# Optimization experiments

Hardware: AMD Instinct MI355X
Metric: run time of the kernel (lower is better)

The kernel has to match this reference:

```python
import jax, jax.numpy as jnp
import numpy as np

K = 1024
H = 16
HEAD = K // H

def setup_inputs() -> dict:
    key = jax.random.key(0)
    ks = jax.random.split(key, 6)
    b, t = 2, 2048
    x = jax.random.normal(ks[0], (b, t, K), dtype=jnp.float32)
    padding = jnp.ones((b, t), dtype=jnp.int32)
    s = 1.0 / np.sqrt(K)
    Wq = jax.random.normal(ks[1], (K, K), dtype=jnp.float32) * s
    Wk = jax.random.normal(ks[2], (K, K), dtype=jnp.float32) * s
    Wv = jax.random.normal(ks[3], (K, K), dtype=jnp.float32) * s
    Wo = jax.random.normal(ks[4], (K, K), dtype=jnp.float32) * s
    bo = jnp.zeros((K,), dtype=jnp.float32)
    return {"x": x, "padding": padding, "Wq": Wq, "Wk": Wk, "Wv": Wv, "Wo": Wo, "bo": bo}

def reference(x, padding, Wq, Wk, Wv, Wo, bo):
    b, t, k = x.shape
    h, d = H, HEAD
    # projections (nn.Linear: x @ W.T), then split heads -> [b,h,t,d]
    q = (x @ Wq.T).reshape(b, t, h, d).transpose(0, 2, 1, 3)
    kk = (x @ Wk.T).reshape(b, t, h, d).transpose(0, 2, 1, 3)
    v = (x @ Wv.T).reshape(b, t, h, d).transpose(0, 2, 1, 3)
    scores = jnp.einsum('bhqd,bhkd->bhqk', q, kk)
    # key-side padding mask: positions with padding==0 get -inf (before scaling,
    # same result since -inf/sqrt(d) == -inf)
    mask = (padding == 0)[:, None, None, :]  # [b,1,1,t]
    scores = jnp.where(mask, -jnp.inf, scores) / np.sqrt(d).astype(np.float32)
    weights = jax.nn.softmax(scores, axis=-1)
    out = jnp.einsum('bhqk,bhkd->bhqd', weights, v)
    out = out.transpose(0, 2, 1, 3).reshape(b, t, h * d)
    return out @ Wo.T + bo
```

## Files before the change

### kernel.cpp

```cpp
#include <hip/hip_runtime.h>
#include <cmath>
#include <stdint.h>

#define K_DIM 1024
#define NH    16
#define HD    64
#define T     2048
#define NTOK  4096
#define NBH   32

typedef __bf16 bf16x8 __attribute__((ext_vector_type(8)));
typedef float  f32x4  __attribute__((ext_vector_type(4)));

__device__ __forceinline__ unsigned short f2bf(float f) {
  union { float f; unsigned u; } v; v.f = f;
  unsigned u = v.u;
  return (unsigned short)((u + 0x7FFFu + ((u >> 16) & 1u)) >> 16);
}
__device__ __forceinline__ unsigned short f2bf_hu(float f) {
  union { float f; unsigned u; } v; v.f = f;
  return (unsigned short)((v.u + 0x8000u) >> 16);
}

__device__ __forceinline__ void gload16(const void* g, void* l) {
  __builtin_amdgcn_global_load_lds(
      (__attribute__((address_space(1))) void*)(g),
      (__attribute__((address_space(3))) void*)(l),
      16, 0, 0);
}

__global__ void convert_kernel(const float* __restrict__ x,
                               const float* __restrict__ Wq,
                               const float* __restrict__ Wk,
                               const float* __restrict__ Wv,
                               const float* __restrict__ Wo,
                               unsigned short* __restrict__ xb,
                               unsigned short* __restrict__ wqkv,
                               unsigned short* __restrict__ wob)
{
  const size_t NX = (size_t)NTOK * K_DIM;
  const size_t NW = (size_t)K_DIM * K_DIM;
  size_t i = ((size_t)blockIdx.x * blockDim.x + threadIdx.x) * 4;
  const float* src; unsigned short* dst; size_t off;
  if (i < NX)             { src = x;  dst = xb;          off = i; }
  else if (i < NX + NW)   { src = Wq; dst = wqkv;        off = i - NX; }
  else if (i < NX + 2*NW) { src = Wk; dst = wqkv + NW;   off = i - NX - NW; }
  else if (i < NX + 3*NW) { src = Wv; dst = wqkv + 2*NW; off = i - NX - 2*NW; }
  else                    { src = Wo; dst = wob;         off = i - NX - 3*NW; }
  float4 v = *(const float4*)(src + off);
  ushort4 o;
  o.x = f2bf(v.x); o.y = f2bf(v.y); o.z = f2bf(v.z); o.w = f2bf(v.w);
  *(ushort4*)(dst + off) = o;
}

template <int MODE, int TM, int TN>
__global__ __launch_bounds__(256, 2)
void gemm_bt(const unsigned short* __restrict__ A,
             const unsigned short* __restrict__ B,
             unsigned short* __restrict__ o_q,
             unsigned short* __restrict__ o_k,
             unsigned short* __restrict__ o_v,
             float* __restrict__ o_f,
             const float* __restrict__ bias)
{
  __shared__ unsigned short Asm[TM * 64];
  __shared__ unsigned short Bsm[TN * 64];
  const int tid  = threadIdx.x;
  const int wave = tid >> 6;
  const int lane = tid & 63;
  const int lq   = lane & 15;
  const int quad = lane >> 4;
  const int bm = blockIdx.x, bn = blockIdx.y;
  const int wm = (wave >> 1) * (TM / 2), wn = (wave & 1) * (TN / 2);
  const int MT = TM / 32, NT = TN / 32;

  f32x4 acc[MT][NT];
#pragma unroll
  for (int i = 0; i < MT; ++i)
#pragma unroll
    for (int j = 0; j < NT; ++j) acc[i][j] = (f32x4){0.f, 0.f, 0.f, 0.f};

  const char* Ab = (const char*)(A + (size_t)bm * TM * K_DIM);
  const char* Bb = (const char*)(B + (size_t)bn * TN * K_DIM);

  for (int k0 = 0; k0 < K_DIM; k0 += 64) {
#pragma unroll
    for (int i = 0; i < MT; ++i) {
      int off   = i * 4096 + wave * 1024 + lane * 16;
      int row   = off >> 7;
      int chunk = (off >> 4) & 7;
      int scol  = (chunk ^ (row & 7)) << 4;
      gload16(Ab + (size_t)row * (K_DIM * 2) + (size_t)k0 * 2 + scol,
              (char*)Asm + off - lane * 16);
    }
#pragma unroll
    for (int i = 0; i < NT; ++i) {
      int off   = i * 4096 + wave * 1024 + lane * 16;
      int row   = off >> 7;
      int chunk = (off >> 4) & 7;
      int scol  = (chunk ^ (row & 7)) << 4;
      gload16(Bb + (size_t)row * (K_DIM * 2) + (size_t)k0 * 2 + scol,
              (char*)Bsm + off - lane * 16);
    }
    __syncthreads();
#pragma unroll
    for (int kk = 0; kk < 64; kk += 32) {
      bf16x8 af[MT], bfr[NT];
#pragma unroll
      for (int mt = 0; mt < MT; ++mt) {
        int row = wm + mt * 16 + lq;
        int sw  = (quad + (kk >> 3)) ^ (row & 7);
        af[mt] = *(const bf16x8*)((const char*)Asm + row * 128 + (sw << 4));
      }
#pragma unroll
      for (int nt = 0; nt < NT; ++nt) {
        int row = wn + nt * 16 + lq;
        int sw  = (quad + (kk >> 3)) ^ (row & 7);
        bfr[nt] = *(const bf16x8*)((const char*)Bsm + row * 128 + (sw << 4));
      }
#pragma unroll
      for (int mt = 0; mt < MT; ++mt)
#pragma unroll
        for (int nt = 0; nt < NT; ++nt)
          acc[mt][nt] = __builtin_amdgcn_mfma_f32_16x16x32_bf16(af[mt], bfr[nt], acc[mt][nt], 0, 0, 0);
    }
    __syncthreads();
  }

#pragma unroll
  for (int mt = 0; mt < MT; ++mt) {
    int mbase = bm * TM + wm + mt * 16 + quad * 4;
#pragma unroll
    for (int nt = 0; nt < NT; ++nt) {
      int n = bn * TN + wn + nt * 16 + lq;
      if (MODE == 1) {
        int which = mbase >> 10, c = mbase & 1023;
        int h = c >> 6, d0 = c & 63;
        int b = n >> 11, t = n & 2047;
        if (which < 2) {
          ushort4 pk;
          pk.x = f2bf(acc[mt][nt][0]); pk.y = f2bf(acc[mt][nt][1]);
          pk.z = f2bf(acc[mt][nt][2]); pk.w = f2bf(acc[mt][nt][3]);
          unsigned short* dst = which ? o_k : o_q;
          *(ushort4*)&dst[((size_t)(b * NH + h) * T + t) * HD + d0] = pk;
        } else {
#pragma unroll
          for (int r = 0; r < 4; ++r)
            o_v[((size_t)(b * NH + h) * HD + d0 + r) * T + t] = f2bf(acc[mt][nt][r]);
        }
      } else {
        float4 bv = *(const float4*)&bias[mbase];
        float4 o;
        o.x = acc[mt][nt][0] + bv.x; o.y = acc[mt][nt][1] + bv.y;
        o.z = acc[mt][nt][2] + bv.z; o.w = acc[mt][nt][3] + bv.w;
        *(float4*)&o_f[(size_t)n * K_DIM + mbase] = o;
      }
    }
  }
}

__global__ __launch_bounds__(256, 2)
void attn_kernel(const unsigned short* __restrict__ Q,
                 const unsigned short* __restrict__ Kb,
                 const unsigned short* __restrict__ Vt,
                 const int* __restrict__ padding,
                 unsigned short* __restrict__ O)
{
  __shared__ unsigned short Ksm[128 * 64];
  __shared__ unsigned short Vsm[64 * 128];
  __shared__ unsigned short Plds[4][32 * 32 * 4];

  const int tid  = threadIdx.x;
  const int wave = tid >> 6;
  const int lane = tid & 63;
  const int lq   = lane & 15;
  const int quad = lane >> 4;
  const int qt = blockIdx.x;
  const int bh = blockIdx.y;
  const int b  = bh >> 4;
  const int h  = bh & 15;
  const int qbase = qt * 128 + wave * 32;

  bf16x8 qf[2][2];
#pragma unroll
  for (int nq = 0; nq < 2; ++nq)
#pragma unroll
    for (int kk = 0; kk < 2; ++kk)
      qf[nq][kk] = *(const bf16x8*)&Q[((size_t)bh * T + qbase + nq * 16 + lq) * HD + kk * 32 + quad * 8];

  f32x4 o_acc[4][2];
#pragma unroll
  for (int md = 0; md < 4; ++md)
#pragma unroll
    for (int nq = 0; nq < 2; ++nq) o_acc[md][nq] = (f32x4){0.f, 0.f, 0.f, 0.f};
  float l_part[2] = {0.f, 0.f};

  const float Cs = 0.18033688011112042f;

  for (int kt = 0; kt < T / 128; ++kt) {
#pragma unroll
    for (int i = 0; i < 4; ++i) {
      int off = i * 4096 + wave * 1024 + lane * 16;
      {
        int row = off >> 7, chunk = (off >> 4) & 7;
        int scol = (chunk ^ (row & 7)) << 4;
        gload16((const char*)Kb + ((size_t)(bh * T + kt * 128 + row) * HD) * 2 + scol,
                (char*)Ksm + off - lane * 16);
      }
      {
        int row = off >> 8, chunk = (off >> 4) & 15;
        int scol = (chunk ^ (row & 15)) << 4;
        gload16((const char*)Vt + ((size_t)(bh * HD + row) * T + (size_t)kt * 128) * 2 + scol,
                (char*)Vsm + off - lane * 16);
      }
    }
    __syncthreads();

    f32x4 st[8][2];
#pragma unroll
    for (int nt = 0; nt < 8; ++nt)
#pragma unroll
      for (int nq = 0; nq < 2; ++nq) st[nt][nq] = (f32x4){0.f, 0.f, 0.f, 0.f};
#pragma unroll
    for (int kk = 0; kk < 2; ++kk) {
#pragma unroll
      for (int nt = 0; nt < 8; ++nt) {
        int row = nt * 16 + lq;
        int sw  = (quad + kk * 4) ^ (row & 7);
        bf16x8 kf = *(const bf16x8*)((const char*)Ksm + row * 128 + (sw << 4));
        st[nt][0] = __builtin_amdgcn_mfma_f32_16x16x32_bf16(kf, qf[0][kk], st[nt][0], 0, 0, 0);
        st[nt][1] = __builtin_amdgcn_mfma_f32_16x16x32_bf16(kf, qf[1][kk], st[nt][1], 0, 0, 0);
      }
    }

#pragma unroll
    for (int nt = 0; nt < 8; ++nt) {
      int4 pd = *(const int4*)&padding[b * T + kt * 128 + nt * 16 + quad * 4];
#pragma unroll
      for (int nq = 0; nq < 2; ++nq) {
        float p0 = pd.x ? __builtin_amdgcn_exp2f(st[nt][nq][0] * Cs) : 0.f;
        float p1 = pd.y ? __builtin_amdgcn_exp2f(st[nt][nq][1] * Cs) : 0.f;
        float p2 = pd.z ? __builtin_amdgcn_exp2f(st[nt][nq][2] * Cs) : 0.f;
        float p3 = pd.w ? __builtin_amdgcn_exp2f(st[nt][nq][3] * Cs) : 0.f;
        l_part[nq] += (p0 + p1) + (p2 + p3);
        ushort4 pk;
        pk.x = f2bf_hu(p0); pk.y = f2bf_hu(p1); pk.z = f2bf_hu(p2); pk.w = f2bf_hu(p3);
        int row = nt * 4 + quad;
        int col = nq * 16 + lq;
        *(ushort4*)&Plds[wave][(row * 32 + col) * 4] = pk;
      }
    }
    asm volatile("s_waitcnt lgkmcnt(0)" ::: "memory");

#pragma unroll
    for (int kk = 0; kk < 4; ++kk) {
      bf16x8 pf[2];
#pragma unroll
      for (int nq = 0; nq < 2; ++nq) {
        int row0 = kk * 8 + quad * 2;
        ushort4 lo = *(const ushort4*)&Plds[wave][((row0    ) * 32 + nq * 16 + lq) * 4];
        ushort4 hi = *(const ushort4*)&Plds[wave][((row0 + 1) * 32 + nq * 16 + lq) * 4];
        union { ushort4 u[2]; bf16x8 v; } cvt;
        cvt.u[0] = lo; cvt.u[1] = hi;
        pf[nq] = cvt.v;
      }
#pragma unroll
      for (int md = 0; md < 4; ++md) {
        int row = md * 16 + lq;
        int sw  = ((kk * 4 + quad) ^ (row & 15)) << 4;
        bf16x8 vf = *(const bf16x8*)((const char*)Vsm + row * 256 + sw);
        o_acc[md][0] = __builtin_amdgcn_mfma_f32_16x16x32_bf16(vf, pf[0], o_acc[md][0], 0, 0, 0);
        o_acc[md][1] = __builtin_amdgcn_mfma_f32_16x16x32_bf16(vf, pf[1], o_acc[md][1], 0, 0, 0);
      }
    }
    __syncthreads();
  }

  float inv[2];
#pragma unroll
  for (int nq = 0; nq < 2; ++nq) {
    float lsum = l_part[nq];
    lsum += __shfl_xor(lsum, 16);
    lsum += __shfl_xor(lsum, 32);
    inv[nq] = (lsum > 0.f) ? 1.f / lsum : 0.f;
  }
#pragma unroll
  for (int md = 0; md < 4; ++md) {
#pragma unroll
    for (int nq = 0; nq < 2; ++nq) {
      int t = qbase + nq * 16 + lq;
      int chan0 = h * HD + md * 16 + quad * 4;
      ushort4 pk;
      pk.x = f2bf(o_acc[md][nq][0] * inv[nq]);
      pk.y = f2bf(o_acc[md][nq][1] * inv[nq]);
      pk.z = f2bf(o_acc[md][nq][2] * inv[nq]);
      pk.w = f2bf(o_acc[md][nq][3] * inv[nq]);
      *(ushort4*)&O[((size_t)(b * T + t)) * K_DIM + chan0] = pk;
    }
  }
}

extern "C" void kernel_launch(void* const* d_in, const int* in_sizes, int n_in,
                              void* d_out, int out_size, void* d_ws, size_t ws_size,
                              hipStream_t stream)
{
  const float* x       = (const float*)d_in[0];
  const int*   padding = (const int*)d_in[1];
  const float* Wq      = (const float*)d_in[2];
  const float* Wk      = (const float*)d_in[3];
  const float* Wv      = (const float*)d_in[4];
  const float* Wo      = (const float*)d_in[5];
  const float* bo      = (const float*)d_in[6];
  float* out = (float*)d_out;

  char* ws = (char*)d_ws;
  unsigned short* xb   = (unsigned short*)(ws);
  unsigned short* wqkv = (unsigned short*)(ws + (8u  << 20));
  unsigned short* wob  = (unsigned short*)(ws + (14u << 20));
  unsigned short* qb   = (unsigned short*)(ws + (16u << 20));
  unsigned short* kb   = (unsigned short*)(ws + (24u << 20));
  unsigned short* vtb  = (unsigned short*)(ws + (32u << 20));
  unsigned short* ab   = (unsigned short*)(ws + (40u << 20));

  convert_kernel<<<8192, 256, 0, stream>>>(x, Wq, Wk, Wv, Wo, xb, wqkv, wob);

  gemm_bt<1, 128, 128><<<dim3(24, 32), 256, 0, stream>>>(wqkv, xb, qb, kb, vtb, nullptr, nullptr);

  attn_kernel<<<dim3(16, 32), 256, 0, stream>>>(qb, kb, vtb, padding, ab);

  gemm_bt<2, 64, 128><<<dim3(16, 32), 256, 0, stream>>>(wob, ab, nullptr, nullptr, nullptr, out, bo);
}
```

Measured before the change: 189.1 us.

## Fold softmax scale into Wq, halve P LDS buffer, swap attention grid order

```diff
diff --git a/kernel.cpp b/kernel.cpp
--- a/kernel.cpp
+++ b/kernel.cpp
@@ -42,14 +42,17 @@
   const size_t NW = (size_t)K_DIM * K_DIM;
   size_t i = ((size_t)blockIdx.x * blockDim.x + threadIdx.x) * 4;
   const float* src; unsigned short* dst; size_t off;
+  float scale = 1.f;
   if (i < NX)             { src = x;  dst = xb;          off = i; }
-  else if (i < NX + NW)   { src = Wq; dst = wqkv;        off = i - NX; }
+  else if (i < NX + NW)   { src = Wq; dst = wqkv;        off = i - NX;
+                            scale = 0.18033688011112042f; }
   else if (i < NX + 2*NW) { src = Wk; dst = wqkv + NW;   off = i - NX - NW; }
   else if (i < NX + 3*NW) { src = Wv; dst = wqkv + 2*NW; off = i - NX - 2*NW; }
   else                    { src = Wo; dst = wob;         off = i - NX - 3*NW; }
   float4 v = *(const float4*)(src + off);
   ushort4 o;
-  o.x = f2bf(v.x); o.y = f2bf(v.y); o.z = f2bf(v.z); o.w = f2bf(v.w);
+  o.x = f2bf(v.x * scale); o.y = f2bf(v.y * scale);
+  o.z = f2bf(v.z * scale); o.w = f2bf(v.w * scale);
   *(ushort4*)(dst + off) = o;
 }
 
@@ -168,15 +171,15 @@
 {
   __shared__ unsigned short Ksm[128 * 64];
   __shared__ unsigned short Vsm[64 * 128];
-  __shared__ unsigned short Plds[4][32 * 32 * 4];
+  __shared__ unsigned short Plds[4][16 * 32 * 4];
 
   const int tid  = threadIdx.x;
   const int wave = tid >> 6;
   const int lane = tid & 63;
   const int lq   = lane & 15;
   const int quad = lane >> 4;
-  const int qt = blockIdx.x;
-  const int bh = blockIdx.y;
+  const int bh = blockIdx.x;
+  const int qt = blockIdx.y;
   const int b  = bh >> 4;
   const int h  = bh & 15;
   const int qbase = qt * 128 + wave * 32;
@@ -194,8 +197,6 @@
 #pragma unroll
     for (int nq = 0; nq < 2; ++nq) o_acc[md][nq] = (f32x4){0.f, 0.f, 0.f, 0.f};
   float l_part[2] = {0.f, 0.f};
-
-  const float Cs = 0.18033688011112042f;
 
   for (int kt = 0; kt < T / 128; ++kt) {
 #pragma unroll
@@ -234,44 +235,50 @@
     }
 
 #pragma unroll
-    for (int nt = 0; nt < 8; ++nt) {
-      int4 pd = *(const int4*)&padding[b * T + kt * 128 + nt * 16 + quad * 4];
-#pragma unroll
-      for (int nq = 0; nq < 2; ++nq) {
-        float p0 = pd.x ? __builtin_amdgcn_exp2f(st[nt][nq][0] * Cs) : 0.f;
-        float p1 = pd.y ? __builtin_amdgcn_exp2f(st[nt][nq][1] * Cs) : 0.f;
-        float p2 = pd.z ? __builtin_amdgcn_exp2f(st[nt][nq][2] * Cs) : 0.f;
-        float p3 = pd.w ? __builtin_amdgcn_exp2f(st[nt][nq][3] * Cs) : 0.f;
-        l_part[nq] += (p0 + p1) + (p2 + p3);
-        ushort4 pk;
-        pk.x = f2bf_hu(p0); pk.y = f2bf_hu(p1); pk.z = f2bf_hu(p2); pk.w = f2bf_hu(p3);
-        int row = nt * 4 + quad;
-        int col = nq * 16 + lq;
-        *(ushort4*)&Plds[wave][(row * 32 + col) * 4] = pk;
-      }
-    }
-    asm volatile("s_waitcnt lgkmcnt(0)" ::: "memory");
-
-#pragma unroll
-    for (int kk = 0; kk < 4; ++kk) {
-      bf16x8 pf[2];
-#pragma unroll
-      for (int nq = 0; nq < 2; ++nq) {
-        int row0 = kk * 8 + quad * 2;
-        ushort4 lo = *(const ushort4*)&Plds[wave][((row0    ) * 32 + nq * 16 + lq) * 4];
-        ushort4 hi = *(const ushort4*)&Plds[wave][((row0 + 1) * 32 + nq * 16 + lq) * 4];
-        union { ushort4 u[2]; bf16x8 v; } cvt;
-        cvt.u[0] = lo; cvt.u[1] = hi;
-        pf[nq] = cvt.v;
-      }
-#pragma unroll
-      for (int md = 0; md < 4; ++md) {
-        int row = md * 16 + lq;
-        int sw  = ((kk * 4 + quad) ^ (row & 15)) << 4;
-        bf16x8 vf = *(const bf16x8*)((const char*)Vsm + row * 256 + sw);
-        o_acc[md][0] = __builtin_amdgcn_mfma_f32_16x16x32_bf16(vf, pf[0], o_acc[md][0], 0, 0, 0);
-        o_acc[md][1] = __builtin_amdgcn_mfma_f32_16x16x32_bf16(vf, pf[1], o_acc[md][1], 0, 0, 0);
-      }
+    for (int half = 0; half < 2; ++half) {
+#pragma unroll
+      for (int nt2 = 0; nt2 < 4; ++nt2) {
+        int nt = half * 4 + nt2;
+        int4 pd = *(const int4*)&padding[b * T + kt * 128 + nt * 16 + quad * 4];
+#pragma unroll
+        for (int nq = 0; nq < 2; ++nq) {
+          float p0 = pd.x ? __builtin_amdgcn_exp2f(st[nt][nq][0]) : 0.f;
+          float p1 = pd.y ? __builtin_amdgcn_exp2f(st[nt][nq][1]) : 0.f;
+          float p2 = pd.z ? __builtin_amdgcn_exp2f(st[nt][nq][2]) : 0.f;
+          float p3 = pd.w ? __builtin_amdgcn_exp2f(st[nt][nq][3]) : 0.f;
+          l_part[nq] += (p0 + p1) + (p2 + p3);
+          ushort4 pk;
+          pk.x = f2bf_hu(p0); pk.y = f2bf_hu(p1); pk.z = f2bf_hu(p2); pk.w = f2bf_hu(p3);
+          int row = nt2 * 4 + quad;
+          int col = nq * 16 + lq;
+          *(ushort4*)&Plds[wave][(row * 32 + col) * 4] = pk;
+        }
+      }
+      asm volatile("s_waitcnt lgkmcnt(0)" ::: "memory");
+
+#pragma unroll
+      for (int kk2 = 0; kk2 < 2; ++kk2) {
+        int kchunk = half * 2 + kk2;
+        bf16x8 pf[2];
+#pragma unroll
+        for (int nq = 0; nq < 2; ++nq) {
+          int row0 = kk2 * 8 + quad * 2;
+          ushort4 lo = *(const ushort4*)&Plds[wave][((row0    ) * 32 + nq * 16 + lq) * 4];
+          ushort4 hi = *(const ushort4*)&Plds[wave][((row0 + 1) * 32 + nq * 16 + lq) * 4];
+          union { ushort4 u[2]; bf16x8 v; } cvt;
+          cvt.u[0] = lo; cvt.u[1] = hi;
+          pf[nq] = cvt.v;
+        }
+#pragma unroll
+        for (int md = 0; md < 4; ++md) {
+          int row = md * 16 + lq;
+          int sw  = ((kchunk * 4 + quad) ^ (row & 15)) << 4;
+          bf16x8 vf = *(const bf16x8*)((const char*)Vsm + row * 256 + sw);
+          o_acc[md][0] = __builtin_amdgcn_mfma_f32_16x16x32_bf16(vf, pf[0], o_acc[md][0], 0, 0, 0);
+          o_acc[md][1] = __builtin_amdgcn_mfma_f32_16x16x32_bf16(vf, pf[1], o_acc[md][1], 0, 0, 0);
+        }
+      }
+      asm volatile("s_waitcnt lgkmcnt(0)" ::: "memory");
     }
     __syncthreads();
   }
@@ -326,7 +333,7 @@
 
   gemm_bt<1, 128, 128><<<dim3(24, 32), 256, 0, stream>>>(wqkv, xb, qb, kb, vtb, nullptr, nullptr);
 
-  attn_kernel<<<dim3(16, 32), 256, 0, stream>>>(qb, kb, vtb, padding, ab);
+  attn_kernel<<<dim3(32, 16), 256, 0, stream>>>(qb, kb, vtb, padding, ab);
 
   gemm_bt<2, 64, 128><<<dim3(16, 32), 256, 0, stream>>>(wob, ab, nullptr, nullptr, nullptr, out, bo);
 }
```

Result: slower. 207.6 us (+9.8%).
